# Optimization experiments

Measured on AMD Instinct MI355X. Metric: run time of the kernel, lower is better.

## Reference

```python
import jax, jax.numpy as jnp
import numpy as np

HEADS = 16

def rotate_half(t):
    t1, t2 = jnp.split(t, 2, axis=-1)
    return jnp.concatenate([-t2, t1], axis=-1)

def apply_rotary_pos_emb(pos, t):
    # pos: [N, hd] broadcasts against t: [B, H, N, hd]
    return t * jnp.cos(pos) + rotate_half(t) * jnp.sin(pos)

def setup_inputs() -> dict:
    key = jax.random.key(0)
    ks = jax.random.split(key, 6)
    B, N, D, H = 2, 2048, 1024, HEADS
    hd = D // H
    s = D ** -0.5
    x = jax.random.normal(ks[0], (B, N, D), jnp.float32)
    context = jax.random.normal(ks[1], (B, N, D), jnp.float32)
    pos_emb = jax.random.normal(ks[2], (N, hd), jnp.float32)
    Wq = jax.random.normal(ks[3], (D, D), jnp.float32) * s
    Wkv = jax.random.normal(ks[4], (D, 2 * D), jnp.float32) * s
    Wout = jax.random.normal(ks[5], (D, D), jnp.float32) * s
    b_out = jnp.zeros((D,), jnp.float32)
    return {"x": x, "context": context, "pos_emb": pos_emb,
            "Wq": Wq, "Wkv": Wkv, "Wout": Wout, "b_out": b_out}

def reference(x, context, pos_emb, Wq, Wkv, Wout, b_out):
    B, N, D = x.shape
    H = HEADS
    hd = D // H
    scale = hd ** -0.5
    # projections: [B,N,D] -> [B,H,N,hd]
    q = (x @ Wq).reshape(B, N, H, hd).transpose(0, 2, 1, 3)
    k, v = jnp.split(context @ Wkv, 2, axis=-1)
    k = k.reshape(B, N, H, hd).transpose(0, 2, 1, 3)
    v = v.reshape(B, N, H, hd).transpose(0, 2, 1, 3)
    # rotary applied to q and k just before scores
    q = apply_rotary_pos_emb(pos_emb, q)
    k = apply_rotary_pos_emb(pos_emb, k)
    dots = jnp.einsum('bhid,bhjd->bhij', q, k) * scale  # [B,H,N,N]
    attn = jax.nn.softmax(dots, axis=-1)
    out = jnp.einsum('bhij,bhjd->bhid', attn, v)
    out = out.transpose(0, 2, 1, 3).reshape(B, N, D)
    return out @ Wout + b_out
```

## Files before the change

### kernel.cpp

```cpp
#include <hip/hip_runtime.h>
#include <math.h>

#define D_MODEL 1024
#define NSEQ    2048
#define NHEADS  16
#define HD      64

typedef __attribute__((ext_vector_type(8))) short bf16x8;
typedef __attribute__((ext_vector_type(4))) float f32x4;

__device__ inline unsigned short f2bf(float x) {
    union { float f; unsigned int u; } a; a.f = x;
    unsigned int r = a.u + 0x7fffu + ((a.u >> 16) & 1u);
    return (unsigned short)(r >> 16);
}
__device__ inline float bf2f(unsigned short b) {
    union { unsigned int u; float f; } a; a.u = ((unsigned int)b) << 16;
    return a.f;
}
__device__ inline unsigned int pack2(unsigned short a, unsigned short b) {
    return (unsigned int)a | ((unsigned int)b << 16);
}
__device__ inline unsigned int cvtpk_bf16(float lo, float hi) {
    unsigned int r;
    asm volatile("v_cvt_pk_bf16_f32 %0, %1, %2" : "=v"(r) : "v"(lo), "v"(hi));
    return r;
}
__device__ inline float fexp2(float x) { return __builtin_amdgcn_exp2f(x); }
__device__ inline void async_load16(const void* g, void* l) {
    __builtin_amdgcn_global_load_lds(
        (const __attribute__((address_space(1))) unsigned int*)g,
        (__attribute__((address_space(3))) unsigned int*)l, 16, 0, 0);
}

#define QSCALE 0.180336880111112f
#define MSHIFT 12.0f

__global__ __launch_bounds__(256) void prep_kernel(
    const float* __restrict__ x, const float* __restrict__ ctx,
    const float* __restrict__ Wq, const float* __restrict__ Wkv,
    const float* __restrict__ Wout, const float* __restrict__ pos,
    unsigned short* __restrict__ AX, unsigned short* __restrict__ AC,
    unsigned short* __restrict__ WQ, unsigned short* __restrict__ WK,
    unsigned short* __restrict__ WO, float* __restrict__ ct,
    float* __restrict__ st)
{
    __shared__ float Ws[32][33];
    const int bid = blockIdx.x, tid = threadIdx.x;
    if (bid < 8192) {
        const float* src = bid < 4096 ? x : ctx;
        unsigned short* dst = bid < 4096 ? AX : AC;
        int m = bid & 4095;
        int kq = tid * 4;
        float4 v = *reinterpret_cast<const float4*>(&src[(size_t)m * 1024 + kq]);
        float vv[4] = {v.x, v.y, v.z, v.w};
        unsigned short h[4];
#pragma unroll
        for (int c = 0; c < 4; ++c) h[c] = f2bf(vv[c]);
        size_t base = (size_t)m * 2048 + kq;
        *reinterpret_cast<uint2*>(&dst[base]) =
            make_uint2(pack2(h[0], h[1]), pack2(h[2], h[3]));
    } else if (bid < 12288) {
        int t = bid - 8192;
        const float* W; unsigned short* Y; int N, tilesx;
        if (t < 1024)      { W = Wq;   Y = WQ; N = 1024; tilesx = 32; }
        else if (t < 3072) { t -= 1024; W = Wkv; Y = WK; N = 2048; tilesx = 64; }
        else               { t -= 3072; W = Wout; Y = WO; N = 1024; tilesx = 32; }
        int n0 = (t % tilesx) * 32, k0 = (t / tilesx) * 32;
        int c = tid & 31, r4 = tid >> 5;
#pragma unroll
        for (int i = 0; i < 4; ++i) {
            int r = r4 * 4 + i;
            Ws[r][c] = W[(size_t)(k0 + r) * N + n0 + c];
        }
        __syncthreads();
#pragma unroll
        for (int i = 0; i < 4; ++i) {
            int nr = r4 * 4 + i;
            Y[(size_t)(n0 + nr) * 2048 + k0 + c] = f2bf(Ws[c][nr]);
        }
    } else {
        int idx = (bid - 12288) * 256 + tid;
        float s, c;
        sincosf(pos[idx], &s, &c);
        ct[idx] = c;
        st[idx] = s;
    }
}

__global__ __launch_bounds__(512) void gemm_qkv(
    const unsigned short* __restrict__ AX, const unsigned short* __restrict__ AC,
    const unsigned short* __restrict__ WQ, const unsigned short* __restrict__ WK,
    unsigned short* __restrict__ Qb, unsigned short* __restrict__ Kb,
    unsigned short* __restrict__ Vt, const float* __restrict__ ct,
    const float* __restrict__ st)
{
    __shared__ unsigned short As[128 * 64];
    __shared__ unsigned short Bs[128 * 64];
    const int tid = threadIdx.x;
    const int l = tid & 63;
    const int wv = tid >> 6;
    const int wr  = wv >> 2;
    const int wch = (wv & 3) >> 1;
    const int whf = wv & 1;
    const int lr_ = l & 15, lg_ = l >> 4;

    const unsigned short *A, *Bt;
    int row0, col0, isQ;
    if (blockIdx.x < 256) {
        A = AX; Bt = WQ; isQ = 1;
        col0 = (blockIdx.x & 7) * 128;
        row0 = (blockIdx.x >> 3) * 128;
    } else {
        int i2 = blockIdx.x - 256;
        A = AC; Bt = WK; isQ = 0;
        int x = i2 & 7, i = i2 >> 3;
        col0 = (x * 2 + (i & 1)) * 128;
        row0 = (i >> 1) * 128;
    }

    f32x4 acc[4][2];
#pragma unroll
    for (int m = 0; m < 4; ++m)
#pragma unroll
        for (int n = 0; n < 2; ++n) acc[m][n] = (f32x4){0.f, 0.f, 0.f, 0.f};

    const int rsub = l >> 3;
    const int chst = (l & 7) ^ rsub;

    for (int k0 = 0; k0 < 1024; k0 += 64) {
        __syncthreads();
#pragma unroll
        for (int t = 0; t < 2; ++t) {
            int ci = wv * 2 + t;
            int row = ci * 8 + rsub;
            async_load16(&A[(size_t)(row0 + row) * 2048 + k0 + chst * 8],
                         &As[ci * 512]);
            async_load16(&Bt[(size_t)(col0 + row) * 2048 + k0 + chst * 8],
                         &Bs[ci * 512]);
        }
        __syncthreads();
#pragma unroll
        for (int ks = 0; ks < 2; ++ks) {
            int ch2 = (lg_ + ks * 4) ^ (lr_ & 7);
            bf16x8 af[4], bfv[2];
#pragma unroll
            for (int m = 0; m < 4; ++m)
                af[m] = *reinterpret_cast<const bf16x8*>(
                    &As[(wr * 64 + m * 16 + lr_) * 64 + ch2 * 8]);
#pragma unroll
            for (int n = 0; n < 2; ++n)
                bfv[n] = *reinterpret_cast<const bf16x8*>(
                    &Bs[(wch * 64 + whf * 16 + n * 32 + lr_) * 64 + ch2 * 8]);
#pragma unroll
            for (int m = 0; m < 4; ++m)
#pragma unroll
                for (int n = 0; n < 2; ++n)
                    acc[m][n] = __builtin_amdgcn_mfma_f32_16x16x32_bf16(
                        af[m], bfv[n], acc[m][n], 0, 0, 0);
        }
    }

    const int colw = col0 + wch * 64;
    if (isQ || colw < 1024) {
        unsigned short* dst = isQ ? Qb : Kb;
        const int hh = colw >> 6;
        const float qs = isQ ? QSCALE : 1.f;
#pragma unroll
        for (int m = 0; m < 4; ++m) {
            int grow0 = row0 + wr * 64 + m * 16 + lg_ * 4;
            int b = grow0 >> 11, nq0 = grow0 & 2047;
#pragma unroll
            for (int j = 0; j < 4; ++j) {
                int nq = nq0 + j;
                int d = whf * 16 + lr_;
                float a = acc[m][0][j], bb = acc[m][1][j];
                float c1 = ct[nq * 64 + d],      s1 = st[nq * 64 + d];
                float c2 = ct[nq * 64 + d + 32], s2 = st[nq * 64 + d + 32];
                size_t obase = (((size_t)b * 16 + hh) * 2048 + nq) * 64;
                dst[obase + d]      = f2bf((a * c1 - bb * s1) * qs);
                dst[obase + d + 32] = f2bf((bb * c2 + a * s2) * qs);
            }
        }
    } else {
        const int hh = (colw - 1024) >> 6;
#pragma unroll
        for (int m = 0; m < 4; ++m) {
            int grow0 = row0 + wr * 64 + m * 16 + lg_ * 4;
            int b = grow0 >> 11, nq0 = grow0 & 2047;
#pragma unroll
            for (int n = 0; n < 2; ++n) {
                int d = whf * 16 + n * 32 + lr_;
                unsigned int w0 = pack2(f2bf(acc[m][n][0]), f2bf(acc[m][n][1]));
                unsigned int w1 = pack2(f2bf(acc[m][n][2]), f2bf(acc[m][n][3]));
                *reinterpret_cast<uint2*>(
                    &Vt[(((size_t)b * 16 + hh) * 64 + d) * 2048 + nq0]) =
                    make_uint2(w0, w1);
            }
        }
    }
}

__global__ __launch_bounds__(256) void gemm_out(
    const unsigned short* __restrict__ A, const unsigned short* __restrict__ Bt,
    const float* __restrict__ bias, float* __restrict__ C)
{
    __shared__ unsigned short As[64 * 64];
    __shared__ unsigned short Bs[64 * 64];
    const int tid = threadIdx.x;
    const int l = tid & 63;
    const int wv = tid >> 6;
    const int wr = wv >> 1;
    const int wp = wv & 1;
    const int lr_ = l & 15, lg_ = l >> 4;
    const int row0 = (blockIdx.x >> 4) * 64;
    const int col0 = (blockIdx.x & 15) * 64;

    f32x4 acc[2][2];
#pragma unroll
    for (int m = 0; m < 2; ++m)
#pragma unroll
        for (int n = 0; n < 2; ++n) acc[m][n] = (f32x4){0.f, 0.f, 0.f, 0.f};

    const int rsub = l >> 3;
    const int chst = (l & 7) ^ rsub;

    for (int k0 = 0; k0 < 1024; k0 += 64) {
        __syncthreads();
#pragma unroll
        for (int t = 0; t < 2; ++t) {
            int ci = wv + 4 * t;
            int row = ci * 8 + rsub;
            async_load16(&A[(size_t)(row0 + row) * 2048 + k0 + chst * 8],
                         &As[ci * 512]);
            async_load16(&Bt[(size_t)(col0 + row) * 2048 + k0 + chst * 8],
                         &Bs[ci * 512]);
        }
        __syncthreads();
#pragma unroll
        for (int ks = 0; ks < 2; ++ks) {
            int ch2 = (lg_ + ks * 4) ^ (lr_ & 7);
            bf16x8 af[2], bfv[2];
#pragma unroll
            for (int m = 0; m < 2; ++m)
                af[m] = *reinterpret_cast<const bf16x8*>(
                    &As[(wr * 32 + m * 16 + lr_) * 64 + ch2 * 8]);
#pragma unroll
            for (int n = 0; n < 2; ++n)
                bfv[n] = *reinterpret_cast<const bf16x8*>(
                    &Bs[(wp * 16 + n * 32 + lr_) * 64 + ch2 * 8]);
#pragma unroll
            for (int m = 0; m < 2; ++m)
#pragma unroll
                for (int n = 0; n < 2; ++n)
                    acc[m][n] = __builtin_amdgcn_mfma_f32_16x16x32_bf16(
                        af[m], bfv[n], acc[m][n], 0, 0, 0);
        }
    }

#pragma unroll
    for (int m = 0; m < 2; ++m) {
        int grow0 = row0 + wr * 32 + m * 16 + lg_ * 4;
#pragma unroll
        for (int n = 0; n < 2; ++n) {
            int gcol = col0 + wp * 16 + n * 32 + lr_;
            float bv = bias[gcol];
#pragma unroll
            for (int j = 0; j < 4; ++j)
                C[(size_t)(grow0 + j) * 1024 + gcol] = acc[m][n][j] + bv;
        }
    }
}

__global__ __launch_bounds__(512) void flash_mfma(
    const unsigned short* __restrict__ Qb, const unsigned short* __restrict__ Kb,
    const unsigned short* __restrict__ Vt, unsigned short* __restrict__ Oa)
{
    __shared__ unsigned short Ks[3][4096];
    __shared__ unsigned short Vs[3][4096];
    __shared__ unsigned short Ps[8][1024];

    const int tid = threadIdx.x;
    const int l = tid & 63;
    const int w = tid >> 6;
    const int lg = l >> 4;
    const int lr = l & 15;
    const int bh = blockIdx.y;
    const int q0 = blockIdx.x * 128;

    bf16x8 qf[2];
    {
        const unsigned short* qp =
            Qb + ((size_t)bh * NSEQ + q0 + w * 16 + lr) * HD + lg * 8;
        qf[0] = *reinterpret_cast<const bf16x8*>(qp);
        qf[1] = *reinterpret_cast<const bf16x8*>(qp + 32);
    }

    f32x4 oacc[4];
#pragma unroll
    for (int j = 0; j < 4; ++j) oacc[j] = (f32x4){0.f, 0.f, 0.f, 0.f};
    float l_i = 0.f;

    unsigned short* pw = Ps[w];

    const int r_  = tid >> 3;
    const int ch_ = (tid & 7) ^ (r_ & 7);
    const unsigned short* kPtr = Kb + ((size_t)bh * NSEQ + r_) * HD + ch_ * 8;
    const unsigned short* vPtr = Vt + ((size_t)bh * HD + r_) * NSEQ + ch_ * 8;

#define STAGE(b) do {                              \
    async_load16(kPtr, &Ks[b][w * 512]);           \
    async_load16(vPtr, &Vs[b][w * 512]);           \
    kPtr += 64 * HD; vPtr += 64;                   \
} while (0)

#define WAITBAR2 do {                                              \
    asm volatile("s_waitcnt vmcnt(2)" ::: "memory");               \
    __builtin_amdgcn_s_barrier();                                  \
    __builtin_amdgcn_sched_barrier(0);                             \
} while (0)

#define COMPUTE(b) do {                                                        \
    f32x4 sacc[4];                                                             \
    _Pragma("unroll")                                                          \
    for (int n = 0; n < 4; ++n)                                                \
        sacc[n] = (f32x4){-MSHIFT, -MSHIFT, -MSHIFT, -MSHIFT};                 \
    __builtin_amdgcn_s_setprio(1);                                             \
    _Pragma("unroll")                                                          \
    for (int ks = 0; ks < 2; ++ks)                                             \
        _Pragma("unroll")                                                      \
        for (int n = 0; n < 4; ++n) {                                          \
            int kr = n * 16 + lr;                                              \
            int ch = (lg + ks * 4) ^ (kr & 7);                                 \
            bf16x8 kf = *reinterpret_cast<const bf16x8*>(                      \
                &Ks[b][kr * 64 + ch * 8]);                                     \
            sacc[n] = __builtin_amdgcn_mfma_f32_16x16x32_bf16(                 \
                kf, qf[ks], sacc[n], 0, 0, 0);                                 \
        }                                                                      \
    __builtin_amdgcn_s_setprio(0);                                             \
    float p[4][4];                                                             \
    float sum = 0.f;                                                           \
    _Pragma("unroll")                                                          \
    for (int n = 0; n < 4; ++n)                                                \
        _Pragma("unroll")                                                      \
        for (int j = 0; j < 4; ++j) {                                          \
            p[n][j] = fexp2(sacc[n][j]);                                       \
            sum += p[n][j];                                                    \
        }                                                                      \
    sum += __shfl_xor(sum, 16);                                                \
    sum += __shfl_xor(sum, 32);                                                \
    l_i += sum;                                                                \
    _Pragma("unroll")                                                          \
    for (int n = 0; n < 4; ++n) {                                              \
        unsigned int u0 = cvtpk_bf16(p[n][0], p[n][1]);                        \
        unsigned int u1 = cvtpk_bf16(p[n][2], p[n][3]);                        \
        int swc = (2 * n + (lg >> 1)) ^ (lr & 7);                              \
        *reinterpret_cast<uint2*>(&pw[lr * 64 + swc * 8 + 4 * (lg & 1)]) =     \
            make_uint2(u0, u1);                                                \
    }                                                                          \
    asm volatile("s_waitcnt lgkmcnt(0)" ::: "memory");                         \
    __builtin_amdgcn_sched_barrier(0);                                         \
    __builtin_amdgcn_s_setprio(1);                                             \
    _Pragma("unroll")                                                          \
    for (int ks = 0; ks < 2; ++ks) {                                           \
        int pch = (lg + 4 * ks) ^ (lr & 7);                                    \
        bf16x8 pf = *reinterpret_cast<const bf16x8*>(                          \
            &pw[lr * 64 + pch * 8]);                                           \
        _Pragma("unroll")                                                      \
        for (int dt = 0; dt < 4; ++dt) {                                       \
            int d = dt * 16 + lr;                                              \
            int ch = (lg + ks * 4) ^ (d & 7);                                  \
            bf16x8 vf = *reinterpret_cast<const bf16x8*>(                      \
                &Vs[b][d * 64 + ch * 8]);                                      \
            oacc[dt] = __builtin_amdgcn_mfma_f32_16x16x32_bf16(                \
                pf, vf, oacc[dt], 0, 0, 0);                                    \
        }                                                                      \
    }                                                                          \
    __builtin_amdgcn_s_setprio(0);                                             \
} while (0)

    STAGE(0);
    for (int base = 0; base < 30; base += 3) {
        STAGE(1); WAITBAR2; COMPUTE(0);
        STAGE(2); WAITBAR2; COMPUTE(1);
        STAGE(0); WAITBAR2; COMPUTE(2);
    }
    STAGE(1); WAITBAR2; COMPUTE(0);
    asm volatile("s_waitcnt vmcnt(0)" ::: "memory");
    __builtin_amdgcn_s_barrier();
    __builtin_amdgcn_sched_barrier(0);
    COMPUTE(1);
#undef STAGE
#undef WAITBAR2
#undef COMPUTE

    const int b = bh >> 4, h = bh & 15;
#pragma unroll
    for (int j = 0; j < 4; ++j) {
        float lj = __shfl(l_i, (l & 48) | (lg * 4 + j));
        float inv = 1.f / lj;
        int nq = q0 + w * 16 + lg * 4 + j;
        size_t rbase = ((size_t)b * NSEQ + nq) * 2048 + h * 64;
#pragma unroll
        for (int dt = 0; dt < 4; ++dt)
            Oa[rbase + dt * 16 + lr] = f2bf(oacc[dt][j] * inv);
    }
}

__global__ __launch_bounds__(256) void sgemm_kernel(
    const float* __restrict__ A, const float* __restrict__ B,
    const float* __restrict__ bias, float* __restrict__ C,
    int M, int N, int K)
{
    __shared__ float As[16][132];
    __shared__ float Bs[16][132];
    const int tid = threadIdx.x;
    const int tr = tid >> 4;
    const int tc = tid & 15;
    const int arow0 = blockIdx.y * 128;
    const int bcol0 = blockIdx.x * 128;
    float acc[8][8];
#pragma unroll
    for (int i = 0; i < 8; ++i)
#pragma unroll
        for (int j = 0; j < 8; ++j) acc[i][j] = 0.f;
    for (int k0 = 0; k0 < K; k0 += 16) {
#pragma unroll
        for (int t = 0; t < 2; ++t) {
            int f = tid + t * 256;
            int row = f >> 2, kg = f & 3;
            float4 av = *reinterpret_cast<const float4*>(
                &A[(size_t)(arow0 + row) * K + k0 + kg * 4]);
            As[kg * 4 + 0][row] = av.x;
            As[kg * 4 + 1][row] = av.y;
            As[kg * 4 + 2][row] = av.z;
            As[kg * 4 + 3][row] = av.w;
        }
#pragma unroll
        for (int t = 0; t < 2; ++t) {
            int f = tid + t * 256;
            int kr = f >> 5, cg = f & 31;
            *reinterpret_cast<float4*>(&Bs[kr][cg * 4]) =
                *reinterpret_cast<const float4*>(
                    &B[(size_t)(k0 + kr) * N + bcol0 + cg * 4]);
        }
        __syncthreads();
#pragma unroll
        for (int kk = 0; kk < 16; ++kk) {
            float a[8], b[8];
            *reinterpret_cast<float4*>(&a[0]) = *reinterpret_cast<const float4*>(&As[kk][tr * 4]);
            *reinterpret_cast<float4*>(&a[4]) = *reinterpret_cast<const float4*>(&As[kk][64 + tr * 4]);
            *reinterpret_cast<float4*>(&b[0]) = *reinterpret_cast<const float4*>(&Bs[kk][tc * 4]);
            *reinterpret_cast<float4*>(&b[4]) = *reinterpret_cast<const float4*>(&Bs[kk][64 + tc * 4]);
#pragma unroll
            for (int i = 0; i < 8; ++i)
#pragma unroll
                for (int j = 0; j < 8; ++j) acc[i][j] = fmaf(a[i], b[j], acc[i][j]);
        }
        __syncthreads();
    }
#pragma unroll
    for (int i = 0; i < 8; ++i) {
        int row = arow0 + ((i < 4) ? (tr * 4 + i) : (64 + tr * 4 + i - 4));
#pragma unroll
        for (int jh = 0; jh < 2; ++jh) {
            int col = bcol0 + ((jh == 0) ? (tc * 4) : (64 + tc * 4));
            float4 v;
            v.x = acc[i][jh * 4 + 0];
            v.y = acc[i][jh * 4 + 1];
            v.z = acc[i][jh * 4 + 2];
            v.w = acc[i][jh * 4 + 3];
            if (bias) {
                v.x += bias[col + 0]; v.y += bias[col + 1];
                v.z += bias[col + 2]; v.w += bias[col + 3];
            }
            *reinterpret_cast<float4*>(&C[(size_t)row * N + col]) = v;
        }
    }
}

__global__ void rope_kernel(float* __restrict__ t, const float* __restrict__ pos,
                            int rowstride)
{
    int idx = blockIdx.x * 256 + threadIdx.x;
    int d = idx & 31;
    int h = (idx >> 5) & (NHEADS - 1);
    int m = idx >> 9;
    int n = m & (NSEQ - 1);
    float p1 = pos[n * HD + d];
    float p2 = pos[n * HD + 32 + d];
    size_t base = (size_t)m * rowstride + h * HD;
    float a = t[base + d];
    float b = t[base + 32 + d];
    float s1, c1, s2, c2;
    sincosf(p1, &s1, &c1);
    sincosf(p2, &s2, &c2);
    t[base + d]      = a * c1 - b * s1;
    t[base + 32 + d] = b * c2 + a * s2;
}

__global__ __launch_bounds__(256) void flash_kernel(
    const float* __restrict__ q, const float* __restrict__ kv,
    float* __restrict__ o)
{
    __shared__ float Qs[64][68];
    __shared__ float Kt[64][68];
    __shared__ float Vs2[64][68];

    const int rb = blockIdx.x;
    const int bh = blockIdx.y;
    const int b = bh >> 4;
    const int h = bh & (NHEADS - 1);
    const int tid = threadIdx.x;
    const int tr = tid >> 4;
    const int tc = tid & 15;

#pragma unroll
    for (int t = 0; t < 4; ++t) {
        int f = tid + t * 256;
        int row = f >> 4, cg = f & 15;
        *reinterpret_cast<float4*>(&Qs[row][cg * 4]) =
            *reinterpret_cast<const float4*>(
                &q[((size_t)(b * NSEQ + rb * 64 + row)) * D_MODEL + h * HD + cg * 4]);
    }

    float m_i[4], l_i[4], oacc[4][4];
#pragma unroll
    for (int i = 0; i < 4; ++i) {
        m_i[i] = -INFINITY; l_i[i] = 0.f;
#pragma unroll
        for (int j = 0; j < 4; ++j) oacc[i][j] = 0.f;
    }

    float (*Ps2)[68] = Kt;

    for (int jt = 0; jt < NSEQ / 64; ++jt) {
        __syncthreads();
#pragma unroll
        for (int t = 0; t < 4; ++t) {
            int f = tid + t * 256;
            int row = f >> 4, cg = f & 15;
            size_t base = ((size_t)(b * NSEQ + jt * 64 + row)) * (2 * D_MODEL) + h * HD + cg * 4;
            float4 kq = *reinterpret_cast<const float4*>(&kv[base]);
            float4 vv = *reinterpret_cast<const float4*>(&kv[base + D_MODEL]);
            Kt[cg * 4 + 0][row] = kq.x;
            Kt[cg * 4 + 1][row] = kq.y;
            Kt[cg * 4 + 2][row] = kq.z;
            Kt[cg * 4 + 3][row] = kq.w;
            *reinterpret_cast<float4*>(&Vs2[row][cg * 4]) = vv;
        }
        __syncthreads();

        float s[4][4];
#pragma unroll
        for (int i = 0; i < 4; ++i)
#pragma unroll
            for (int j = 0; j < 4; ++j) s[i][j] = 0.f;
        for (int dg = 0; dg < 16; ++dg) {
            float Qv[4][4];
#pragma unroll
            for (int i = 0; i < 4; ++i)
                *reinterpret_cast<float4*>(Qv[i]) =
                    *reinterpret_cast<const float4*>(&Qs[tr * 4 + i][dg * 4]);
#pragma unroll
            for (int dd = 0; dd < 4; ++dd) {
                float ka[4];
                *reinterpret_cast<float4*>(ka) =
                    *reinterpret_cast<const float4*>(&Kt[dg * 4 + dd][tc * 4]);
#pragma unroll
                for (int i = 0; i < 4; ++i)
#pragma unroll
                    for (int j = 0; j < 4; ++j)
                        s[i][j] = fmaf(Qv[i][dd], ka[j], s[i][j]);
            }
        }

#pragma unroll
        for (int i = 0; i < 4; ++i) {
            float tmax = -INFINITY;
#pragma unroll
            for (int j = 0; j < 4; ++j) {
                s[i][j] *= 0.125f;
                tmax = fmaxf(tmax, s[i][j]);
            }
#pragma unroll
            for (int msk = 1; msk < 16; msk <<= 1)
                tmax = fmaxf(tmax, __shfl_xor(tmax, msk, 16));
            float mnew = fmaxf(m_i[i], tmax);
            float corr = expf(m_i[i] - mnew);
            float tsum = 0.f;
#pragma unroll
            for (int j = 0; j < 4; ++j) {
                s[i][j] = expf(s[i][j] - mnew);
                tsum += s[i][j];
            }
#pragma unroll
            for (int msk = 1; msk < 16; msk <<= 1)
                tsum += __shfl_xor(tsum, msk, 16);
            l_i[i] = l_i[i] * corr + tsum;
            m_i[i] = mnew;
#pragma unroll
            for (int j = 0; j < 4; ++j) oacc[i][j] *= corr;
        }

        __syncthreads();
#pragma unroll
        for (int i = 0; i < 4; ++i) {
            float4 v;
            v.x = s[i][0]; v.y = s[i][1]; v.z = s[i][2]; v.w = s[i][3];
            *reinterpret_cast<float4*>(&Ps2[tr * 4 + i][tc * 4]) = v;
        }
        __syncthreads();

        for (int cg = 0; cg < 16; ++cg) {
            float P_[4][4], V_[4][4];
#pragma unroll
            for (int i = 0; i < 4; ++i)
                *reinterpret_cast<float4*>(P_[i]) =
                    *reinterpret_cast<const float4*>(&Ps2[tr * 4 + i][cg * 4]);
#pragma unroll
            for (int c = 0; c < 4; ++c)
                *reinterpret_cast<float4*>(V_[c]) =
                    *reinterpret_cast<const float4*>(&Vs2[cg * 4 + c][tc * 4]);
#pragma unroll
            for (int i = 0; i < 4; ++i)
#pragma unroll
                for (int c = 0; c < 4; ++c)
#pragma unroll
                    for (int j = 0; j < 4; ++j)
                        oacc[i][j] = fmaf(P_[i][c], V_[c][j], oacc[i][j]);
        }
    }

#pragma unroll
    for (int i = 0; i < 4; ++i) {
        float inv = 1.f / l_i[i];
        float4 v;
        v.x = oacc[i][0] * inv; v.y = oacc[i][1] * inv;
        v.z = oacc[i][2] * inv; v.w = oacc[i][3] * inv;
        *reinterpret_cast<float4*>(
            &o[((size_t)(b * NSEQ + rb * 64 + tr * 4 + i)) * D_MODEL + h * HD + tc * 4]) = v;
    }
}

extern "C" void kernel_launch(void* const* d_in, const int* in_sizes, int n_in,
                              void* d_out, int out_size, void* d_ws, size_t ws_size,
                              hipStream_t stream) {
    const float* x       = (const float*)d_in[0];
    const float* context = (const float*)d_in[1];
    const float* pos     = (const float*)d_in[2];
    const float* Wq      = (const float*)d_in[3];
    const float* Wkv     = (const float*)d_in[4];
    const float* Wout    = (const float*)d_in[5];
    const float* b_out   = (const float*)d_in[6];
    float* out = (float*)d_out;

    const int M = 2 * NSEQ;
    dim3 blk(256);

    const size_t NEED = 76546048ULL;
    if (ws_size >= NEED) {
        unsigned short* AX = (unsigned short*)d_ws;
        unsigned short* AC = AX + 8388608;
        unsigned short* WQ = AC + 8388608;
        unsigned short* WK = WQ + 2097152;
        unsigned short* WO = WK + 4194304;
        unsigned short* Qb = WO + 2097152;
        unsigned short* Kb = Qb + 4194304;
        unsigned short* Vt = Kb + 4194304;
        float* ct = (float*)(Vt + 4194304);
        float* st = ct + 131072;

        prep_kernel<<<12800, blk, 0, stream>>>(
            x, context, Wq, Wkv, Wout, pos, AX, AC, WQ, WK, WO, ct, st);
        gemm_qkv<<<768, dim3(512), 0, stream>>>(AX, AC, WQ, WK, Qb, Kb, Vt, ct, st);
        flash_mfma<<<dim3(NSEQ / 128, 32), dim3(512), 0, stream>>>(Qb, Kb, Vt, AX);
        gemm_out<<<1024, blk, 0, stream>>>(AX, WO, b_out, out);
    } else {
        float* ws = (float*)d_ws;
        float* q  = ws;
        float* kv = q + (size_t)M * D_MODEL;
        float* o  = kv + (size_t)M * 2 * D_MODEL;
        sgemm_kernel<<<dim3(D_MODEL / 128, M / 128), blk, 0, stream>>>(
            x, Wq, nullptr, q, M, D_MODEL, D_MODEL);
        sgemm_kernel<<<dim3(2 * D_MODEL / 128, M / 128), blk, 0, stream>>>(
            context, Wkv, nullptr, kv, M, 2 * D_MODEL, D_MODEL);
        rope_kernel<<<(M * NHEADS * 32) / 256, blk, 0, stream>>>(q, pos, D_MODEL);
        rope_kernel<<<(M * NHEADS * 32) / 256, blk, 0, stream>>>(kv, pos, 2 * D_MODEL);
        flash_kernel<<<dim3(NSEQ / 64, 2 * NHEADS), blk, 0, stream>>>(q, kv, o);
        sgemm_kernel<<<dim3(D_MODEL / 128, M / 128), blk, 0, stream>>>(
            o, Wout, b_out, out, M, D_MODEL, D_MODEL);
    }
}
```

Baseline: 118.0 us.

## Software-pipeline flash attention: overlap next QK^T with softmax and PV over four buffers

Splits the per-tile attention body into QK, softmax and PV phases and reorders them so the QK^T MFMAs for the next key tile are issued before the PV of the current tile. Ping-pong score registers (sA/sB) carry the scores across iterations, and K/V LDS staging grows from three to four buffers. The aim is to hide exp/softmax latency and LDS waits behind matrix-core work. In exchange it uses more LDS and registers, which could lower occupancy, and the tail schedule with its barrier counts must be exactly right.

```diff
diff --git a/kernel.cpp b/kernel.cpp
--- a/kernel.cpp
+++ b/kernel.cpp
@@ -276,8 +276,8 @@
     const unsigned short* __restrict__ Qb, const unsigned short* __restrict__ Kb,
     const unsigned short* __restrict__ Vt, unsigned short* __restrict__ Oa)
 {
-    __shared__ unsigned short Ks[3][4096];
-    __shared__ unsigned short Vs[3][4096];
+    __shared__ unsigned short Ks[4][4096];
+    __shared__ unsigned short Vs[4][4096];
     __shared__ unsigned short Ps[8][1024];
 
     const int tid = threadIdx.x;
@@ -300,6 +300,7 @@
 #pragma unroll
     for (int j = 0; j < 4; ++j) oacc[j] = (f32x4){0.f, 0.f, 0.f, 0.f};
     float l_i = 0.f;
+    f32x4 sA[4], sB[4];
 
     unsigned short* pw = Ps[w];
 
@@ -314,17 +315,22 @@
     kPtr += 64 * HD; vPtr += 64;                   \
 } while (0)
 
-#define WAITBAR2 do {                                              \
+#define BAR2 do {                                                  \
     asm volatile("s_waitcnt vmcnt(2)" ::: "memory");               \
     __builtin_amdgcn_s_barrier();                                  \
     __builtin_amdgcn_sched_barrier(0);                             \
 } while (0)
 
-#define COMPUTE(b) do {                                                        \
-    f32x4 sacc[4];                                                             \
+#define BAR0 do {                                                  \
+    asm volatile("s_waitcnt vmcnt(0)" ::: "memory");               \
+    __builtin_amdgcn_s_barrier();                                  \
+    __builtin_amdgcn_sched_barrier(0);                             \
+} while (0)
+
+#define QK(b, SACC) do {                                                       \
     _Pragma("unroll")                                                          \
     for (int n = 0; n < 4; ++n)                                                \
-        sacc[n] = (f32x4){-MSHIFT, -MSHIFT, -MSHIFT, -MSHIFT};                 \
+        SACC[n] = (f32x4){-MSHIFT, -MSHIFT, -MSHIFT, -MSHIFT};                 \
     __builtin_amdgcn_s_setprio(1);                                             \
     _Pragma("unroll")                                                          \
     for (int ks = 0; ks < 2; ++ks)                                             \
@@ -334,17 +340,20 @@
             int ch = (lg + ks * 4) ^ (kr & 7);                                 \
             bf16x8 kf = *reinterpret_cast<const bf16x8*>(                      \
                 &Ks[b][kr * 64 + ch * 8]);                                     \
-            sacc[n] = __builtin_amdgcn_mfma_f32_16x16x32_bf16(                 \
-                kf, qf[ks], sacc[n], 0, 0, 0);                                 \
+            SACC[n] = __builtin_amdgcn_mfma_f32_16x16x32_bf16(                 \
+                kf, qf[ks], SACC[n], 0, 0, 0);                                 \
         }                                                                      \
     __builtin_amdgcn_s_setprio(0);                                             \
+} while (0)
+
+#define SM(SACC) do {                                                          \
     float p[4][4];                                                             \
     float sum = 0.f;                                                           \
     _Pragma("unroll")                                                          \
     for (int n = 0; n < 4; ++n)                                                \
         _Pragma("unroll")                                                      \
         for (int j = 0; j < 4; ++j) {                                          \
-            p[n][j] = fexp2(sacc[n][j]);                                       \
+            p[n][j] = fexp2(SACC[n][j]);                                       \
             sum += p[n][j];                                                    \
         }                                                                      \
     sum += __shfl_xor(sum, 16);                                                \
@@ -358,6 +367,9 @@
         *reinterpret_cast<uint2*>(&pw[lr * 64 + swc * 8 + 4 * (lg & 1)]) =     \
             make_uint2(u0, u1);                                                \
     }                                                                          \
+} while (0)
+
+#define PV(b) do {                                                             \
     asm volatile("s_waitcnt lgkmcnt(0)" ::: "memory");                         \
     __builtin_amdgcn_sched_barrier(0);                                         \
     __builtin_amdgcn_s_setprio(1);                                             \
@@ -379,20 +391,31 @@
     __builtin_amdgcn_s_setprio(0);                                             \
 } while (0)
 
-    STAGE(0);
-    for (int base = 0; base < 30; base += 3) {
-        STAGE(1); WAITBAR2; COMPUTE(0);
-        STAGE(2); WAITBAR2; COMPUTE(1);
-        STAGE(0); WAITBAR2; COMPUTE(2);
-    }
-    STAGE(1); WAITBAR2; COMPUTE(0);
-    asm volatile("s_waitcnt vmcnt(0)" ::: "memory");
-    __builtin_amdgcn_s_barrier();
+    STAGE(0); STAGE(1);
+    BAR2;
+    QK(0, sA);
+    STAGE(2);
+    BAR2;
+
+    for (int it = 0; it < 7; ++it) {
+        STAGE(3); SM(sA); QK(1, sB); PV(0); BAR2;
+        STAGE(0); SM(sB); QK(2, sA); PV(1); BAR2;
+        STAGE(1); SM(sA); QK(3, sB); PV(2); BAR2;
+        STAGE(2); SM(sB); QK(0, sA); PV(3); BAR2;
+    }
+    STAGE(3); SM(sA); QK(1, sB); PV(0); BAR2;
+    SM(sB); QK(2, sA); PV(1); BAR0;
+    SM(sA); QK(3, sB); PV(2); BAR0;
+    SM(sB);
+    asm volatile("s_waitcnt lgkmcnt(0)" ::: "memory");
     __builtin_amdgcn_sched_barrier(0);
-    COMPUTE(1);
+    PV(3);
 #undef STAGE
-#undef WAITBAR2
-#undef COMPUTE
+#undef BAR2
+#undef BAR0
+#undef QK
+#undef SM
+#undef PV
 
     const int b = bh >> 4, h = bh & 15;
 #pragma unroll
```

Measured after the change: 119.7 us. About the same (+1.5%).

## Shrink flash blocks to 256 threads, double-buffer K/V, compute row sums via MFMA

Applied to the files above, without the earlier changes.

The flash attention kernel now uses 256-thread blocks covering 64 queries each, which doubles the grid. The K/V ring goes from three buffers to two, with full vmcnt(0) waits and __syncthreads between tiles. Each thread issues two async loads per tensor per stage to cover the 64-row tile. The softmax denominator is no longer summed with exp-sum shuffles; an extra MFMA of P against a ones vector accumulates it, trading shuffle and ALU work for one extra matrix op per k-step. The shallower prefetch and stricter waits may expose more memory latency, while the smaller blocks and lower LDS use could raise occupancy.

```diff
diff --git a/kernel.cpp b/kernel.cpp
--- a/kernel.cpp
+++ b/kernel.cpp
@@ -272,13 +272,13 @@
     }
 }
 
-__global__ __launch_bounds__(512) void flash_mfma(
+__global__ __launch_bounds__(256) void flash_mfma(
     const unsigned short* __restrict__ Qb, const unsigned short* __restrict__ Kb,
     const unsigned short* __restrict__ Vt, unsigned short* __restrict__ Oa)
 {
-    __shared__ unsigned short Ks[3][4096];
-    __shared__ unsigned short Vs[3][4096];
-    __shared__ unsigned short Ps[8][1024];
+    __shared__ unsigned short Ks[2][4096];
+    __shared__ unsigned short Vs[2][4096];
+    __shared__ unsigned short Ps[4][1024];
 
     const int tid = threadIdx.x;
     const int l = tid & 63;
@@ -286,7 +286,7 @@
     const int lg = l >> 4;
     const int lr = l & 15;
     const int bh = blockIdx.y;
-    const int q0 = blockIdx.x * 128;
+    const int q0 = blockIdx.x * 64;
 
     bf16x8 qf[2];
     {
@@ -296,10 +296,14 @@
         qf[1] = *reinterpret_cast<const bf16x8*>(qp + 32);
     }
 
-    f32x4 oacc[4];
+    f32x4 oacc[4], lacc;
 #pragma unroll
     for (int j = 0; j < 4; ++j) oacc[j] = (f32x4){0.f, 0.f, 0.f, 0.f};
-    float l_i = 0.f;
+    lacc = (f32x4){0.f, 0.f, 0.f, 0.f};
+
+    bf16x8 ones;
+#pragma unroll
+    for (int i = 0; i < 8; ++i) ones[i] = (short)0x3F80;
 
     unsigned short* pw = Ps[w];
 
@@ -308,16 +312,12 @@
     const unsigned short* kPtr = Kb + ((size_t)bh * NSEQ + r_) * HD + ch_ * 8;
     const unsigned short* vPtr = Vt + ((size_t)bh * HD + r_) * NSEQ + ch_ * 8;
 
-#define STAGE(b) do {                              \
-    async_load16(kPtr, &Ks[b][w * 512]);           \
-    async_load16(vPtr, &Vs[b][w * 512]);           \
-    kPtr += 64 * HD; vPtr += 64;                   \
-} while (0)
-
-#define WAITBAR2 do {                                              \
-    asm volatile("s_waitcnt vmcnt(2)" ::: "memory");               \
-    __builtin_amdgcn_s_barrier();                                  \
-    __builtin_amdgcn_sched_barrier(0);                             \
+#define STAGE(b) do {                                        \
+    async_load16(kPtr,             &Ks[b][w * 512]);         \
+    async_load16(kPtr + 32 * HD,   &Ks[b][w * 512 + 2048]);  \
+    async_load16(vPtr,             &Vs[b][w * 512]);         \
+    async_load16(vPtr + 32 * NSEQ, &Vs[b][w * 512 + 2048]);  \
+    kPtr += 64 * HD; vPtr += 64;                             \
 } while (0)
 
 #define COMPUTE(b) do {                                                        \
@@ -339,17 +339,11 @@
         }                                                                      \
     __builtin_amdgcn_s_setprio(0);                                             \
     float p[4][4];                                                             \
-    float sum = 0.f;                                                           \
     _Pragma("unroll")                                                          \
     for (int n = 0; n < 4; ++n)                                                \
         _Pragma("unroll")                                                      \
-        for (int j = 0; j < 4; ++j) {                                          \
+        for (int j = 0; j < 4; ++j)                                            \
             p[n][j] = fexp2(sacc[n][j]);                                       \
-            sum += p[n][j];                                                    \
-        }                                                                      \
-    sum += __shfl_xor(sum, 16);                                                \
-    sum += __shfl_xor(sum, 32);                                                \
-    l_i += sum;                                                                \
     _Pragma("unroll")                                                          \
     for (int n = 0; n < 4; ++n) {                                              \
         unsigned int u0 = cvtpk_bf16(p[n][0], p[n][1]);                        \
@@ -375,30 +369,33 @@
             oacc[dt] = __builtin_amdgcn_mfma_f32_16x16x32_bf16(                \
                 pf, vf, oacc[dt], 0, 0, 0);                                    \
         }                                                                      \
+        lacc = __builtin_amdgcn_mfma_f32_16x16x32_bf16(                        \
+            pf, ones, lacc, 0, 0, 0);                                          \
     }                                                                          \
     __builtin_amdgcn_s_setprio(0);                                             \
 } while (0)
 
     STAGE(0);
-    for (int base = 0; base < 30; base += 3) {
-        STAGE(1); WAITBAR2; COMPUTE(0);
-        STAGE(2); WAITBAR2; COMPUTE(1);
-        STAGE(0); WAITBAR2; COMPUTE(2);
-    }
-    STAGE(1); WAITBAR2; COMPUTE(0);
     asm volatile("s_waitcnt vmcnt(0)" ::: "memory");
-    __builtin_amdgcn_s_barrier();
-    __builtin_amdgcn_sched_barrier(0);
-    COMPUTE(1);
+    __syncthreads();
+
+    for (int jt = 0; jt < NSEQ / 64; jt += 2) {
+        STAGE(1);
+        COMPUTE(0);
+        asm volatile("s_waitcnt vmcnt(0)" ::: "memory");
+        __syncthreads();
+        if (jt + 2 < NSEQ / 64) STAGE(0);
+        COMPUTE(1);
+        asm volatile("s_waitcnt vmcnt(0)" ::: "memory");
+        __syncthreads();
+    }
 #undef STAGE
-#undef WAITBAR2
 #undef COMPUTE
 
     const int b = bh >> 4, h = bh & 15;
 #pragma unroll
     for (int j = 0; j < 4; ++j) {
-        float lj = __shfl(l_i, (l & 48) | (lg * 4 + j));
-        float inv = 1.f / lj;
+        float inv = 1.f / lacc[j];
         int nq = q0 + w * 16 + lg * 4 + j;
         size_t rbase = ((size_t)b * NSEQ + nq) * 2048 + h * 64;
 #pragma unroll
@@ -674,7 +671,7 @@
         prep_kernel<<<12800, blk, 0, stream>>>(
             x, context, Wq, Wkv, Wout, pos, AX, AC, WQ, WK, WO, ct, st);
         gemm_qkv<<<768, dim3(512), 0, stream>>>(AX, AC, WQ, WK, Qb, Kb, Vt, ct, st);
-        flash_mfma<<<dim3(NSEQ / 128, 32), dim3(512), 0, stream>>>(Qb, Kb, Vt, AX);
+        flash_mfma<<<dim3(NSEQ / 64, 32), blk, 0, stream>>>(Qb, Kb, Vt, AX);
         gemm_out<<<1024, blk, 0, stream>>>(AX, WO, b_out, out);
     } else {
         float* ws = (float*)d_ws;
```

Result: slower. 126.5 us (+7.2%).
